# Kernel optimization log

Hardware: AMD Instinct MI355X
Metric: run time of the kernel (lower is better)

Reference implementation:

```python
import jax, jax.numpy as jnp
import numpy as np

N_NODES = 8192
D_FEAT = 256


def setup_inputs() -> dict:
    key = jax.random.key(0)
    k1, k2, k3, k4, k5 = jax.random.split(key, 5)
    X = jax.random.normal(k1, (N_NODES, D_FEAT), dtype=jnp.float32)
    # Dense normalized adjacency-like matrix (A_hat); scale by 1/N for stable magnitudes.
    A_hat = jax.random.uniform(k2, (N_NODES, N_NODES), dtype=jnp.float32) / N_NODES
    w_global = jax.random.uniform(k3, (1,), dtype=jnp.float32)
    w_local = jax.random.uniform(k4, (N_NODES,), dtype=jnp.float32)
    W_agg = jax.random.normal(k5, (D_FEAT, D_FEAT), dtype=jnp.float32) / np.sqrt(D_FEAT)
    return {"X": X, "A_hat": A_hat, "w_global": w_global, "w_local": w_local, "W_agg": W_agg}


def reference(X, A_hat, w_global, w_local, W_agg):
    # GCN-style aggregation: f(X, A_hat) = A_hat @ X @ W_agg, then ReLU.
    agg = jax.nn.relu((A_hat @ X) @ W_agg)  # [n, d]
    # xi = sigmoid(w_global) * diag(sigmoid(w_local)); diagonal => elementwise row scale.
    s = (jax.nn.sigmoid(w_global) * jax.nn.sigmoid(w_local))[:, None]  # [n, 1]
    # xi @ agg + (I - xi) @ X  ==  s*agg + X - s*X, fused in one pass.
    return s * agg + X - s * X
```

## Files before the change

kernel.cpp:

```cpp
#include <hip/hip_runtime.h>
#include <hip/hip_bf16.h>


typedef __attribute__((ext_vector_type(4))) float f32x4;
typedef __attribute__((ext_vector_type(8))) __bf16 bf16x8;
typedef __attribute__((ext_vector_type(8))) unsigned short u16x8;

#define GLOBAL_AS __attribute__((address_space(1)))
#define LDS_AS __attribute__((address_space(3)))

static __device__ __forceinline__ void gload16(const void* g, void* l) {
  __builtin_amdgcn_global_load_lds((const GLOBAL_AS void*)g, (LDS_AS void*)l, 16, 0, 0);
}
static __device__ __forceinline__ void gload16_stream(const void* g, void* l) {
  __builtin_amdgcn_global_load_lds((const GLOBAL_AS void*)g, (LDS_AS void*)l, 16, 0, 0x12);
}

static __device__ __forceinline__ unsigned short f2bf_bits(float f) {
  __bf16 h = (__bf16)f;
  return __builtin_bit_cast(unsigned short, h);
}
static __device__ __forceinline__ float bf2f(unsigned short u) {
  return __builtin_bit_cast(float, (unsigned)u << 16);
}

__global__ void prep_kernel(const float* __restrict__ W,
                            const float* __restrict__ wg,
                            const float* __restrict__ wl,
                            unsigned short* __restrict__ WT,
                            float* __restrict__ s) {
  int tid = blockIdx.x * 256 + threadIdx.x;
  int k = tid >> 8, n = tid & 255;
  float w = W[tid];
  int kt = k >> 5, kloc = k & 31;
  WT[kt * 8192 + n * 32 + kloc] = f2bf_bits(w);
  if (tid < 8192) {
    float sg = 1.0f / (1.0f + expf(-wg[0]));
    float sl = 1.0f / (1.0f + expf(-wl[tid]));
    s[tid] = sg * sl;
  }
}

__global__ __launch_bounds__(256, 2) void gemm_xw(
    const float* __restrict__ X,
    const unsigned short* __restrict__ WT,
    unsigned short* __restrict__ XWT2) {
  __shared__ float As[2][32 * 32];
  __shared__ unsigned short Bs[2][128 * 32];

  const int bm = blockIdx.x & 255;
  const int bn = blockIdx.x >> 8;
  const int m0 = bm * 32;
  const int tid = threadIdx.x;
  const int w = tid >> 6;
  const int l = tid & 63;
  const int lr = l & 15;
  const int lq = l >> 4;

  const int pA = w * 1024 + l * 16;
  const int rA = pA >> 7;
  const int qA = (pA >> 4) & 7;
  const int ssA = qA ^ (rA & 7);
  const char* Asrc0 = (const char*)X + (size_t)(m0 + rA) * 1024 + ssA * 16;
  const char* Bsrc0 = (const char*)WT + bn * 8192 + w * 2048 + l * 16;

  f32x4 acc[2][2];
#pragma unroll
  for (int i = 0; i < 2; ++i)
#pragma unroll
    for (int j = 0; j < 2; ++j) acc[i][j] = (f32x4){0.f, 0.f, 0.f, 0.f};

  auto stage = [&](int t, int buf) {
    gload16(Asrc0 + (size_t)t * 128, (char*)&As[buf][0] + w * 1024);
    const char* bs = Bsrc0 + (size_t)t * 16384;
    gload16(bs, (char*)&Bs[buf][0] + w * 2048);
    gload16(bs + 1024, (char*)&Bs[buf][0] + w * 2048 + 1024);
  };

  auto compute = [&](int buf) {
    bf16x8 af[2];
#pragma unroll
    for (int mi = 0; mi < 2; ++mi) {
      int r = mi * 16 + lr;
      const float* ap = &As[buf][r * 32];
      int s0 = (2 * lq) ^ (r & 7);
      int s1 = (2 * lq + 1) ^ (r & 7);
      f32x4 a0 = *(const f32x4*)(ap + s0 * 4);
      f32x4 a1 = *(const f32x4*)(ap + s1 * 4);
      bf16x8 v;
      v[0] = (__bf16)a0.x; v[1] = (__bf16)a0.y; v[2] = (__bf16)a0.z; v[3] = (__bf16)a0.w;
      v[4] = (__bf16)a1.x; v[5] = (__bf16)a1.y; v[6] = (__bf16)a1.z; v[7] = (__bf16)a1.w;
      af[mi] = v;
    }
    bf16x8 bfr[2];
#pragma unroll
    for (int ni = 0; ni < 2; ++ni) {
      int row = w * 32 + ni * 16 + lr;
      bfr[ni] = *(const bf16x8*)(&Bs[buf][row * 32 + lq * 8]);
    }
#pragma unroll
    for (int mi = 0; mi < 2; ++mi)
#pragma unroll
      for (int ni = 0; ni < 2; ++ni)
        acc[mi][ni] = __builtin_amdgcn_mfma_f32_16x16x32_bf16(af[mi], bfr[ni], acc[mi][ni], 0, 0, 0);
  };

  stage(0, 0);
  __syncthreads();
  for (int t = 0; t < 8; ++t) {
    int cur = t & 1;
    if (t + 1 < 8) stage(t + 1, cur ^ 1);
    compute(cur);
    __syncthreads();
  }

#pragma unroll
  for (int mi = 0; mi < 2; ++mi)
#pragma unroll
    for (int ni2 = 0; ni2 < 2; ++ni2) {
      f32x4 z = acc[mi][ni2];
      int n = bn * 128 + w * 32 + ni2 * 16 + lr;
      int k = bm * 32 + mi * 16 + lq * 4;
      int c = k >> 6;
      int kk = (k >> 5) & 1;
      int ni = (n >> 4) & 1;
      int wp = n >> 5;
      int lane2 = (n & 15) + 16 * ((k >> 3) & 3);
      int j0 = k & 7;
      size_t off = (((size_t)c * 8 + wp) * 4 + kk * 2 + ni) * 512 + lane2 * 8 + j0;
      ushort4 u;
      u.x = f2bf_bits(z[0]); u.y = f2bf_bits(z[1]);
      u.z = f2bf_bits(z[2]); u.w = f2bf_bits(z[3]);
      *(ushort4*)(XWT2 + off) = u;
    }
}

__global__ __launch_bounds__(512, 4) void gemm_ks8(
    const float* __restrict__ A,
    const unsigned short* __restrict__ B2,
    unsigned short* __restrict__ P) {
  __shared__ unsigned short Al[2][8 * 512];

  const int bid = blockIdx.x;
  const int mtile = bid >> 3, kseg = bid & 7;
  const int m0 = mtile * 128;
  const int tid = threadIdx.x;
  const int w = tid >> 6, l = tid & 63;
  const int lr = l & 15, lq = l >> 4;

  const int r = tid >> 2, c4 = tid & 3;
  const float* gA = A + (size_t)(m0 + r) * 8192 + kseg * 1024 + c4 * 8;
  const int woff = (r >> 4) * 512 + ((r & 15) + 16 * c4) * 8;

  const unsigned short* Bbase = B2 + (size_t)kseg * 262144 + l * 8;

  f32x4 acc[8][2];
#pragma unroll
  for (int i = 0; i < 8; ++i)
#pragma unroll
    for (int j = 0; j < 2; ++j) acc[i][j] = (f32x4){0.f, 0.f, 0.f, 0.f};

  f32x4 sa0, sa1;
  bf16x8 Bf0, Bf1;

  auto loadA = [&](int h) {
    sa0 = *(const f32x4*)(gA + h * 32);
    sa1 = *(const f32x4*)(gA + h * 32 + 4);
  };
  auto writeA = [&](int h) {
    bf16x8 b;
    b[0] = (__bf16)sa0.x; b[1] = (__bf16)sa0.y; b[2] = (__bf16)sa0.z; b[3] = (__bf16)sa0.w;
    b[4] = (__bf16)sa1.x; b[5] = (__bf16)sa1.y; b[6] = (__bf16)sa1.z; b[7] = (__bf16)sa1.w;
    *(bf16x8*)(&Al[h & 1][woff]) = b;
  };
  auto loadB = [&](int h) {
    const unsigned short* p = Bbase + ((((h >> 1) * 8 + w) * 4 + (h & 1) * 2) << 9);
    Bf0 = *(const bf16x8*)(p);
    Bf1 = *(const bf16x8*)(p + 512);
  };
  auto compute = [&](int h) {
    const unsigned short* Ab = &Al[h & 1][0];
#pragma unroll
    for (int mi = 0; mi < 8; ++mi) {
      bf16x8 af = *(const bf16x8*)(Ab + mi * 512 + l * 8);
      acc[mi][0] = __builtin_amdgcn_mfma_f32_16x16x32_bf16(af, Bf0, acc[mi][0], 0, 0, 0);
      acc[mi][1] = __builtin_amdgcn_mfma_f32_16x16x32_bf16(af, Bf1, acc[mi][1], 0, 0, 0);
    }
  };

  loadA(0);
  writeA(0);
  loadB(0);
  loadA(1);
  asm volatile("s_waitcnt lgkmcnt(0)" ::: "memory");
  asm volatile("s_barrier" ::: "memory");

  for (int h = 0; h < 31; ++h) {
    compute(h);
    loadB(h + 1);
    writeA(h + 1);
    if (h < 30) loadA(h + 2);
    asm volatile("s_waitcnt lgkmcnt(0)" ::: "memory");
    asm volatile("s_barrier" ::: "memory");
  }
  compute(31);

  unsigned short* Pb = P + (size_t)kseg * (8192 * 256);
#pragma unroll
  for (int mi = 0; mi < 8; ++mi)
#pragma unroll
    for (int ni = 0; ni < 2; ++ni) {
      f32x4 z = acc[mi][ni];
      int n = w * 32 + ni * 16 + lr;
#pragma unroll
      for (int i = 0; i < 4; ++i) {
        int m = m0 + mi * 16 + lq * 4 + i;
        Pb[(size_t)m * 256 + n] = f2bf_bits(z[i]);
      }
    }
}

__global__ __launch_bounds__(256) void finalize8(
    const unsigned short* __restrict__ P,
    const float* __restrict__ X,
    const float* __restrict__ s,
    float* __restrict__ out) {
  int i = blockIdx.x * 256 + threadIdx.x;
  int m = i >> 5;
  float acc[8] = {0.f, 0.f, 0.f, 0.f, 0.f, 0.f, 0.f, 0.f};
#pragma unroll
  for (int ks = 0; ks < 8; ++ks) {
    u16x8 v = *(const u16x8*)(P + (size_t)ks * 2097152 + (size_t)i * 8);
#pragma unroll
    for (int j = 0; j < 8; ++j) acc[j] += bf2f(v[j]);
  }
  float sv = s[m];
  f32x4 x0 = *(const f32x4*)(X + (size_t)i * 8);
  f32x4 x1 = *(const f32x4*)(X + (size_t)i * 8 + 4);
  f32x4 o0, o1;
#pragma unroll
  for (int j = 0; j < 4; ++j) {
    o0[j] = x0[j] + sv * (fmaxf(acc[j], 0.f) - x0[j]);
    o1[j] = x1[j] + sv * (fmaxf(acc[4 + j], 0.f) - x1[j]);
  }
  *(f32x4*)(out + (size_t)i * 8) = o0;
  *(f32x4*)(out + (size_t)i * 8 + 4) = o1;
}

template <int NT, bool SPLIT>
__global__ __launch_bounds__(512, 4) void gemm_main(
    const float* __restrict__ A,
    const unsigned short* __restrict__ B2,
    const float* __restrict__ X,
    const float* __restrict__ s,
    float* __restrict__ out,
    float* __restrict__ P) {
  __shared__ float As[4][32 * 64];

  const int bid = blockIdx.x;
  const int m0 = SPLIT ? (bid >> 1) * 32 : bid * 32;
  const int khalf = SPLIT ? (bid & 1) : 0;
  const int tid = threadIdx.x;
  const int w = tid >> 6;
  const int l = tid & 63;
  const int lr = l & 15;
  const int lq = l >> 4;

  const int rA = tid >> 4;
  const int qA = tid & 15;
  const int sqA = qA ^ (rA & 15);
  const char* Asrc =
      (const char*)A + (size_t)(m0 + rA) * 32768 + (size_t)khalf * 16384 + sqA * 16;
  const char* Bbase =
      (const char*)B2 + (size_t)khalf * 64 * 32768 + (size_t)w * 4096 + (size_t)l * 16;

  f32x4 acc[2][2];
#pragma unroll
  for (int i = 0; i < 2; ++i)
#pragma unroll
    for (int j = 0; j < 2; ++j) acc[i][j] = (f32x4){0.f, 0.f, 0.f, 0.f};

  struct BF { bf16x8 a, b, c, d; };
  BF Bf0, Bf1;

  auto stageA = [&](int h, int buf) {
    gload16_stream(Asrc + (size_t)h * 256, (char*)&As[buf][0] + w * 1024);
  };
  auto loadB = [&](int h, BF& f) {
    const char* p = Bbase + (size_t)h * 32768;
    f.a = *(const bf16x8*)(p);
    f.b = *(const bf16x8*)(p + 1024);
    f.c = *(const bf16x8*)(p + 2048);
    f.d = *(const bf16x8*)(p + 3072);
  };

  auto compute = [&](int buf, const BF& f) {
    const char* Ab = (const char*)&As[buf][0];
    bf16x8 af[2][2];
#pragma unroll
    for (int kk = 0; kk < 2; ++kk)
#pragma unroll
      for (int mi = 0; mi < 2; ++mi) {
        int rr = mi * 16 + lr;
        int s0 = (kk * 8 + 2 * lq) ^ (rr & 15);
        int s1 = ((kk * 8 + 2 * lq) + 1) ^ (rr & 15);
        f32x4 a0 = *(const f32x4*)(Ab + rr * 256 + s0 * 16);
        f32x4 a1 = *(const f32x4*)(Ab + rr * 256 + s1 * 16);
        bf16x8 v;
        v[0] = (__bf16)a0.x; v[1] = (__bf16)a0.y; v[2] = (__bf16)a0.z; v[3] = (__bf16)a0.w;
        v[4] = (__bf16)a1.x; v[5] = (__bf16)a1.y; v[6] = (__bf16)a1.z; v[7] = (__bf16)a1.w;
        af[kk][mi] = v;
      }
    acc[0][0] = __builtin_amdgcn_mfma_f32_16x16x32_bf16(af[0][0], f.a, acc[0][0], 0, 0, 0);
    acc[0][1] = __builtin_amdgcn_mfma_f32_16x16x32_bf16(af[0][0], f.b, acc[0][1], 0, 0, 0);
    acc[1][0] = __builtin_amdgcn_mfma_f32_16x16x32_bf16(af[0][1], f.a, acc[1][0], 0, 0, 0);
    acc[1][1] = __builtin_amdgcn_mfma_f32_16x16x32_bf16(af[0][1], f.b, acc[1][1], 0, 0, 0);
    acc[0][0] = __builtin_amdgcn_mfma_f32_16x16x32_bf16(af[1][0], f.c, acc[0][0], 0, 0, 0);
    acc[0][1] = __builtin_amdgcn_mfma_f32_16x16x32_bf16(af[1][0], f.d, acc[0][1], 0, 0, 0);
    acc[1][0] = __builtin_amdgcn_mfma_f32_16x16x32_bf16(af[1][1], f.c, acc[1][0], 0, 0, 0);
    acc[1][1] = __builtin_amdgcn_mfma_f32_16x16x32_bf16(af[1][1], f.d, acc[1][1], 0, 0, 0);
  };

  stageA(0, 0);
  loadB(0, Bf0);
  stageA(1, 1);
  loadB(1, Bf1);
  stageA(2, 2);
  stageA(3, 3);

  for (int h = 0; h < NT - 4; h += 2) {
    asm volatile("s_waitcnt vmcnt(6)" ::: "memory");
    asm volatile("s_barrier" ::: "memory");
    compute(h & 3, Bf0);
    asm volatile("s_waitcnt lgkmcnt(0)" ::: "memory");
    asm volatile("s_barrier" ::: "memory");
    loadB(h + 2, Bf0);
    stageA(h + 4, h & 3);

    asm volatile("s_waitcnt vmcnt(6)" ::: "memory");
    asm volatile("s_barrier" ::: "memory");
    compute((h + 1) & 3, Bf1);
    asm volatile("s_waitcnt lgkmcnt(0)" ::: "memory");
    asm volatile("s_barrier" ::: "memory");
    loadB(h + 3, Bf1);
    stageA(h + 5, (h + 1) & 3);
  }
  asm volatile("s_waitcnt vmcnt(6)" ::: "memory");
  asm volatile("s_barrier" ::: "memory");
  compute(0, Bf0);
  asm volatile("s_waitcnt lgkmcnt(0)" ::: "memory");
  asm volatile("s_barrier" ::: "memory");
  loadB(NT - 2, Bf0);

  asm volatile("s_waitcnt vmcnt(5)" ::: "memory");
  asm volatile("s_barrier" ::: "memory");
  compute(1, Bf1);
  asm volatile("s_waitcnt lgkmcnt(0)" ::: "memory");
  asm volatile("s_barrier" ::: "memory");
  loadB(NT - 1, Bf1);

  asm volatile("s_waitcnt vmcnt(4)" ::: "memory");
  asm volatile("s_barrier" ::: "memory");
  compute(2, Bf0);
  asm volatile("s_waitcnt lgkmcnt(0)" ::: "memory");
  asm volatile("s_barrier" ::: "memory");

  asm volatile("s_waitcnt vmcnt(0)" ::: "memory");
  asm volatile("s_barrier" ::: "memory");
  compute(3, Bf1);

  if (SPLIT) {
    float* Pb = P + (size_t)khalf * 8192 * 256;
#pragma unroll
    for (int mi = 0; mi < 2; ++mi)
#pragma unroll
      for (int ni = 0; ni < 2; ++ni) {
        f32x4 z = acc[mi][ni];
        int n = w * 32 + ni * 16 + lr;
#pragma unroll
        for (int i = 0; i < 4; ++i) {
          int m = m0 + mi * 16 + lq * 4 + i;
          Pb[m * 256 + n] = z[i];
        }
      }
  } else {
#pragma unroll
    for (int mi = 0; mi < 2; ++mi)
#pragma unroll
      for (int ni = 0; ni < 2; ++ni) {
        f32x4 z = acc[mi][ni];
        int n = w * 32 + ni * 16 + lr;
#pragma unroll
        for (int i = 0; i < 4; ++i) {
          int m = m0 + mi * 16 + lq * 4 + i;
          float x = X[m * 256 + n];
          float sv = s[m];
          out[m * 256 + n] = x + sv * (fmaxf(z[i], 0.f) - x);
        }
      }
  }
}

__global__ __launch_bounds__(256) void finalize_kernel(
    const float* __restrict__ P,
    const float* __restrict__ X,
    const float* __restrict__ s,
    float* __restrict__ out) {
  int i = blockIdx.x * 256 + threadIdx.x;
  int m = i >> 6;
  f32x4 p0 = *(const f32x4*)(P + (size_t)i * 4);
  f32x4 p1 = *(const f32x4*)(P + 2097152 + (size_t)i * 4);
  f32x4 x = *(const f32x4*)(X + (size_t)i * 4);
  float sv = s[m];
  f32x4 o;
#pragma unroll
  for (int j = 0; j < 4; ++j) o[j] = x[j] + sv * (fmaxf(p0[j] + p1[j], 0.f) - x[j]);
  *(f32x4*)(out + (size_t)i * 4) = o;
}

extern "C" void kernel_launch(void* const* d_in, const int* in_sizes, int n_in,
                              void* d_out, int out_size, void* d_ws, size_t ws_size,
                              hipStream_t stream) {
  const float* X = (const float*)d_in[0];
  const float* A = (const float*)d_in[1];
  const float* wg = (const float*)d_in[2];
  const float* wl = (const float*)d_in[3];
  const float* W = (const float*)d_in[4];
  float* out = (float*)d_out;

  unsigned short* XWT2 = (unsigned short*)d_ws;
  unsigned short* WT = (unsigned short*)((char*)d_ws + 4194304);
  float* s = (float*)((char*)d_ws + 4194304 + 131072);
  char* Pbase = (char*)d_ws + 4194304 + 131072 + 32768;

  prep_kernel<<<256, 256, 0, stream>>>(W, wg, wl, WT, s);
  gemm_xw<<<512, 256, 0, stream>>>(X, WT, XWT2);

  const size_t head = 4194304 + 131072 + 32768;
  const size_t need8 = head + (size_t)8 * 8192 * 256 * 2;
  const size_t need2 = head + (size_t)2 * 8192 * 256 * 4;
  if (ws_size >= need8) {
    gemm_ks8<<<512, 512, 0, stream>>>(A, XWT2, (unsigned short*)Pbase);
    finalize8<<<1024, 256, 0, stream>>>((const unsigned short*)Pbase, X, s, out);
  } else if (ws_size >= need2) {
    gemm_main<64, true><<<512, 512, 0, stream>>>(A, XWT2, X, s, out, (float*)Pbase);
    finalize_kernel<<<2048, 256, 0, stream>>>((const float*)Pbase, X, s, out);
  } else {
    gemm_main<128, false><<<256, 512, 0, stream>>>(A, XWT2, X, s, out, nullptr);
  }
}
```

Measured before the change: 103.4 us.

## Double K-step per barrier in split-K GEMM and stagger half the blocks

The split-K GEMM main loop now handles a 64-wide K chunk per iteration instead of 32. It doubles the LDS A tile, gives each thread four float4 loads, and interleaves two half-computes with separate B fragment prefetches, which halves the number of barriers. Separately, blocks with bit 256 of the block index sleep briefly at start, staggering memory traffic. The cost is more LDS and registers per block, which could lower occupancy under launch_bounds(512,4).

```diff
diff --git a/kernel.cpp b/kernel.cpp
--- a/kernel.cpp
+++ b/kernel.cpp
@@ -139,7 +139,7 @@
     const float* __restrict__ A,
     const unsigned short* __restrict__ B2,
     unsigned short* __restrict__ P) {
-  __shared__ unsigned short Al[2][8 * 512];
+  __shared__ unsigned short Al[2][16 * 512];
 
   const int bid = blockIdx.x;
   const int mtile = bid >> 3, kseg = bid & 7;
@@ -148,9 +148,12 @@
   const int w = tid >> 6, l = tid & 63;
   const int lr = l & 15, lq = l >> 4;
 
+  if (bid & 256) __builtin_amdgcn_s_sleep(32);
+
   const int r = tid >> 2, c4 = tid & 3;
-  const float* gA = A + (size_t)(m0 + r) * 8192 + kseg * 1024 + c4 * 8;
-  const int woff = (r >> 4) * 512 + ((r & 15) + 16 * c4) * 8;
+  const float* gA = A + (size_t)(m0 + r) * 8192 + kseg * 1024 + c4 * 16;
+  const int ks = c4 >> 1, kq0 = (c4 & 1) * 2;
+  const int woff0 = (ks * 8 + (r >> 4)) * 512 + ((r & 15) + 16 * kq0) * 8;
 
   const unsigned short* Bbase = B2 + (size_t)kseg * 262144 + l * 8;
 
@@ -160,50 +163,65 @@
 #pragma unroll
     for (int j = 0; j < 2; ++j) acc[i][j] = (f32x4){0.f, 0.f, 0.f, 0.f};
 
-  f32x4 sa0, sa1;
-  bf16x8 Bf0, Bf1;
+  f32x4 sa0, sa1, sa2, sa3;
+  bf16x8 BfA0, BfA1, BfB0, BfB1;
 
   auto loadA = [&](int h) {
-    sa0 = *(const f32x4*)(gA + h * 32);
-    sa1 = *(const f32x4*)(gA + h * 32 + 4);
+    const float* p = gA + h * 64;
+    sa0 = *(const f32x4*)(p);
+    sa1 = *(const f32x4*)(p + 4);
+    sa2 = *(const f32x4*)(p + 8);
+    sa3 = *(const f32x4*)(p + 12);
   };
   auto writeA = [&](int h) {
-    bf16x8 b;
-    b[0] = (__bf16)sa0.x; b[1] = (__bf16)sa0.y; b[2] = (__bf16)sa0.z; b[3] = (__bf16)sa0.w;
-    b[4] = (__bf16)sa1.x; b[5] = (__bf16)sa1.y; b[6] = (__bf16)sa1.z; b[7] = (__bf16)sa1.w;
-    *(bf16x8*)(&Al[h & 1][woff]) = b;
-  };
-  auto loadB = [&](int h) {
-    const unsigned short* p = Bbase + ((((h >> 1) * 8 + w) * 4 + (h & 1) * 2) << 9);
-    Bf0 = *(const bf16x8*)(p);
-    Bf1 = *(const bf16x8*)(p + 512);
-  };
-  auto compute = [&](int h) {
-    const unsigned short* Ab = &Al[h & 1][0];
+    bf16x8 b0, b1;
+    b0[0] = (__bf16)sa0.x; b0[1] = (__bf16)sa0.y; b0[2] = (__bf16)sa0.z; b0[3] = (__bf16)sa0.w;
+    b0[4] = (__bf16)sa1.x; b0[5] = (__bf16)sa1.y; b0[6] = (__bf16)sa1.z; b0[7] = (__bf16)sa1.w;
+    b1[0] = (__bf16)sa2.x; b1[1] = (__bf16)sa2.y; b1[2] = (__bf16)sa2.z; b1[3] = (__bf16)sa2.w;
+    b1[4] = (__bf16)sa3.x; b1[5] = (__bf16)sa3.y; b1[6] = (__bf16)sa3.z; b1[7] = (__bf16)sa3.w;
+    *(bf16x8*)(&Al[h & 1][woff0]) = b0;
+    *(bf16x8*)(&Al[h & 1][woff0 + 128]) = b1;
+  };
+  auto loadBA = [&](int h) {
+    const unsigned short* p = Bbase + (((h * 8 + w) * 4 + 0) << 9);
+    BfA0 = *(const bf16x8*)(p);
+    BfA1 = *(const bf16x8*)(p + 512);
+  };
+  auto loadBB = [&](int h) {
+    const unsigned short* p = Bbase + (((h * 8 + w) * 4 + 2) << 9);
+    BfB0 = *(const bf16x8*)(p);
+    BfB1 = *(const bf16x8*)(p + 512);
+  };
+  auto computeHalf = [&](int buf, int ksel, const bf16x8& F0, const bf16x8& F1) {
+    const unsigned short* Ab = &Al[buf][ksel * 4096];
 #pragma unroll
     for (int mi = 0; mi < 8; ++mi) {
       bf16x8 af = *(const bf16x8*)(Ab + mi * 512 + l * 8);
-      acc[mi][0] = __builtin_amdgcn_mfma_f32_16x16x32_bf16(af, Bf0, acc[mi][0], 0, 0, 0);
-      acc[mi][1] = __builtin_amdgcn_mfma_f32_16x16x32_bf16(af, Bf1, acc[mi][1], 0, 0, 0);
+      acc[mi][0] = __builtin_amdgcn_mfma_f32_16x16x32_bf16(af, F0, acc[mi][0], 0, 0, 0);
+      acc[mi][1] = __builtin_amdgcn_mfma_f32_16x16x32_bf16(af, F1, acc[mi][1], 0, 0, 0);
     }
   };
 
   loadA(0);
   writeA(0);
-  loadB(0);
+  loadBA(0);
+  loadBB(0);
   loadA(1);
   asm volatile("s_waitcnt lgkmcnt(0)" ::: "memory");
   asm volatile("s_barrier" ::: "memory");
 
-  for (int h = 0; h < 31; ++h) {
-    compute(h);
-    loadB(h + 1);
+  for (int h = 0; h < 15; ++h) {
+    computeHalf(h & 1, 0, BfA0, BfA1);
+    loadBA(h + 1);
+    computeHalf(h & 1, 1, BfB0, BfB1);
+    loadBB(h + 1);
     writeA(h + 1);
-    if (h < 30) loadA(h + 2);
+    if (h < 14) loadA(h + 2);
     asm volatile("s_waitcnt lgkmcnt(0)" ::: "memory");
     asm volatile("s_barrier" ::: "memory");
   }
-  compute(31);
+  computeHalf(1, 0, BfA0, BfA1);
+  computeHalf(1, 1, BfB0, BfB1);
 
   unsigned short* Pb = P + (size_t)kseg * (8192 * 256);
 #pragma unroll
```

After: 106.9 us. +3.3%, slower.

## Warp-specialize A@XW GEMM into producer/consumer waves with 8-slot LDS ring

Applied to the files above, without the earlier changes.

Replaces the split-K-by-8 GEMM with a 768-thread kernel where 4 producer waves stream fp32 A with nontemporal loads, convert it to bf16 and fill an 8-slot LDS ring, while 8 consumer waves run MFMAs. Split-K drops from 8 to 4, so the grid is 256 blocks and the bf16 partial buffer and finalize reads are halved. The aim is to overlap A streaming with compute and cut partial-sum traffic. In exchange there are fewer blocks in flight and more LDS and registers per block, and the B operand is now loaded inside the compute step rather than prefetched.

```diff
diff --git a/kernel.cpp b/kernel.cpp
--- a/kernel.cpp
+++ b/kernel.cpp
@@ -135,92 +135,109 @@
     }
 }
 
-__global__ __launch_bounds__(512, 4) void gemm_ks8(
+__global__ __launch_bounds__(768, 3) void gemm_pc(
     const float* __restrict__ A,
     const unsigned short* __restrict__ B2,
     unsigned short* __restrict__ P) {
-  __shared__ unsigned short Al[2][8 * 512];
+  __shared__ unsigned short ring[8 * 4096];
 
   const int bid = blockIdx.x;
-  const int mtile = bid >> 3, kseg = bid & 7;
+  const int mtile = bid >> 2, kseg = bid & 3;
   const int m0 = mtile * 128;
   const int tid = threadIdx.x;
-  const int w = tid >> 6, l = tid & 63;
+  const bool consumer = tid < 512;
+  const int w = tid >> 6;
+  const int l = tid & 63;
   const int lr = l & 15, lq = l >> 4;
 
-  const int r = tid >> 2, c4 = tid & 3;
-  const float* gA = A + (size_t)(m0 + r) * 8192 + kseg * 1024 + c4 * 8;
-  const int woff = (r >> 4) * 512 + ((r & 15) + 16 * c4) * 8;
-
-  const unsigned short* Bbase = B2 + (size_t)kseg * 262144 + l * 8;
-
   f32x4 acc[8][2];
 #pragma unroll
   for (int i = 0; i < 8; ++i)
 #pragma unroll
     for (int j = 0; j < 2; ++j) acc[i][j] = (f32x4){0.f, 0.f, 0.f, 0.f};
 
-  f32x4 sa0, sa1;
-  bf16x8 Bf0, Bf1;
-
-  auto loadA = [&](int h) {
-    sa0 = *(const f32x4*)(gA + h * 32);
-    sa1 = *(const f32x4*)(gA + h * 32 + 4);
-  };
-  auto writeA = [&](int h) {
-    bf16x8 b;
-    b[0] = (__bf16)sa0.x; b[1] = (__bf16)sa0.y; b[2] = (__bf16)sa0.z; b[3] = (__bf16)sa0.w;
-    b[4] = (__bf16)sa1.x; b[5] = (__bf16)sa1.y; b[6] = (__bf16)sa1.z; b[7] = (__bf16)sa1.w;
-    *(bf16x8*)(&Al[h & 1][woff]) = b;
-  };
-  auto loadB = [&](int h) {
-    const unsigned short* p = Bbase + ((((h >> 1) * 8 + w) * 4 + (h & 1) * 2) << 9);
-    Bf0 = *(const bf16x8*)(p);
-    Bf1 = *(const bf16x8*)(p + 512);
-  };
-  auto compute = [&](int h) {
-    const unsigned short* Ab = &Al[h & 1][0];
+  const int p = tid - 512;
+  const int prow = (p & 255) >> 1;
+  const int pk16 = (p & 1) * 16;
+  const float* gA =
+      A + (size_t)(m0 + prow) * 8192 + (size_t)kseg * 2048 + pk16;
+  const int pwoff = (prow >> 4) * 512 + ((prow & 15) + 16 * ((p & 1) * 2)) * 8;
+
+  auto stage_super = [&](int j) {
+    f32x4 v[16];
+#pragma unroll
+    for (int s2 = 0; s2 < 4; ++s2) {
+      const float* src = gA + (size_t)(4 * j + s2) * 32;
+#pragma unroll
+      for (int i = 0; i < 4; ++i)
+        v[s2 * 4 + i] = __builtin_nontemporal_load((const f32x4*)(src + i * 4));
+    }
+#pragma unroll
+    for (int s2 = 0; s2 < 4; ++s2) {
+      int hh = 4 * j + s2;
+      unsigned short* dst = &ring[(hh & 7) * 4096 + pwoff];
+      bf16x8 b0, b1;
+      b0[0] = (__bf16)v[s2 * 4 + 0].x; b0[1] = (__bf16)v[s2 * 4 + 0].y;
+      b0[2] = (__bf16)v[s2 * 4 + 0].z; b0[3] = (__bf16)v[s2 * 4 + 0].w;
+      b0[4] = (__bf16)v[s2 * 4 + 1].x; b0[5] = (__bf16)v[s2 * 4 + 1].y;
+      b0[6] = (__bf16)v[s2 * 4 + 1].z; b0[7] = (__bf16)v[s2 * 4 + 1].w;
+      b1[0] = (__bf16)v[s2 * 4 + 2].x; b1[1] = (__bf16)v[s2 * 4 + 2].y;
+      b1[2] = (__bf16)v[s2 * 4 + 2].z; b1[3] = (__bf16)v[s2 * 4 + 2].w;
+      b1[4] = (__bf16)v[s2 * 4 + 3].x; b1[5] = (__bf16)v[s2 * 4 + 3].y;
+      b1[6] = (__bf16)v[s2 * 4 + 3].z; b1[7] = (__bf16)v[s2 * 4 + 3].w;
+      *(bf16x8*)(dst) = b0;
+      *(bf16x8*)(dst + 128) = b1;
+    }
+  };
+
+  auto compute_slot = [&](int hh) {
+    int c = kseg * 32 + (hh >> 1);
+    const unsigned short* bp =
+        B2 + ((((size_t)c * 8 + w) * 4 + (size_t)(hh & 1) * 2) << 9) + l * 8;
+    bf16x8 B0 = *(const bf16x8*)(bp);
+    bf16x8 B1 = *(const bf16x8*)(bp + 512);
+    const unsigned short* Ab = &ring[(hh & 7) * 4096];
 #pragma unroll
     for (int mi = 0; mi < 8; ++mi) {
       bf16x8 af = *(const bf16x8*)(Ab + mi * 512 + l * 8);
-      acc[mi][0] = __builtin_amdgcn_mfma_f32_16x16x32_bf16(af, Bf0, acc[mi][0], 0, 0, 0);
-      acc[mi][1] = __builtin_amdgcn_mfma_f32_16x16x32_bf16(af, Bf1, acc[mi][1], 0, 0, 0);
-    }
-  };
-
-  loadA(0);
-  writeA(0);
-  loadB(0);
-  loadA(1);
+      acc[mi][0] = __builtin_amdgcn_mfma_f32_16x16x32_bf16(af, B0, acc[mi][0], 0, 0, 0);
+      acc[mi][1] = __builtin_amdgcn_mfma_f32_16x16x32_bf16(af, B1, acc[mi][1], 0, 0, 0);
+    }
+  };
+
+  if (!consumer) stage_super(0);
   asm volatile("s_waitcnt lgkmcnt(0)" ::: "memory");
   asm volatile("s_barrier" ::: "memory");
 
-  for (int h = 0; h < 31; ++h) {
-    compute(h);
-    loadB(h + 1);
-    writeA(h + 1);
-    if (h < 30) loadA(h + 2);
+  for (int sp = 0; sp < 16; ++sp) {
+    if (consumer) {
+#pragma unroll
+      for (int jj = 0; jj < 4; ++jj) compute_slot(sp * 4 + jj);
+    } else {
+      if (sp < 15) stage_super(sp + 1);
+    }
     asm volatile("s_waitcnt lgkmcnt(0)" ::: "memory");
     asm volatile("s_barrier" ::: "memory");
   }
-  compute(31);
-
-  unsigned short* Pb = P + (size_t)kseg * (8192 * 256);
-#pragma unroll
-  for (int mi = 0; mi < 8; ++mi)
-#pragma unroll
-    for (int ni = 0; ni < 2; ++ni) {
-      f32x4 z = acc[mi][ni];
-      int n = w * 32 + ni * 16 + lr;
-#pragma unroll
-      for (int i = 0; i < 4; ++i) {
-        int m = m0 + mi * 16 + lq * 4 + i;
-        Pb[(size_t)m * 256 + n] = f2bf_bits(z[i]);
+
+  if (consumer) {
+    unsigned short* Pb = P + (size_t)kseg * (8192 * 256);
+#pragma unroll
+    for (int mi = 0; mi < 8; ++mi)
+#pragma unroll
+      for (int ni = 0; ni < 2; ++ni) {
+        f32x4 z = acc[mi][ni];
+        int n = w * 32 + ni * 16 + lr;
+#pragma unroll
+        for (int i = 0; i < 4; ++i) {
+          int m = m0 + mi * 16 + lq * 4 + i;
+          Pb[(size_t)m * 256 + n] = f2bf_bits(z[i]);
+        }
       }
-    }
-}
-
-__global__ __launch_bounds__(256) void finalize8(
+  }
+}
+
+__global__ __launch_bounds__(256) void finalize4(
     const unsigned short* __restrict__ P,
     const float* __restrict__ X,
     const float* __restrict__ s,
@@ -229,7 +246,7 @@
   int m = i >> 5;
   float acc[8] = {0.f, 0.f, 0.f, 0.f, 0.f, 0.f, 0.f, 0.f};
 #pragma unroll
-  for (int ks = 0; ks < 8; ++ks) {
+  for (int ks = 0; ks < 4; ++ks) {
     u16x8 v = *(const u16x8*)(P + (size_t)ks * 2097152 + (size_t)i * 8);
 #pragma unroll
     for (int j = 0; j < 8; ++j) acc[j] += bf2f(v[j]);
@@ -437,11 +454,11 @@
   gemm_xw<<<512, 256, 0, stream>>>(X, WT, XWT2);
 
   const size_t head = 4194304 + 131072 + 32768;
-  const size_t need8 = head + (size_t)8 * 8192 * 256 * 2;
+  const size_t need4 = head + (size_t)4 * 8192 * 256 * 2;
   const size_t need2 = head + (size_t)2 * 8192 * 256 * 4;
-  if (ws_size >= need8) {
-    gemm_ks8<<<512, 512, 0, stream>>>(A, XWT2, (unsigned short*)Pbase);
-    finalize8<<<1024, 256, 0, stream>>>((const unsigned short*)Pbase, X, s, out);
+  if (ws_size >= need4) {
+    gemm_pc<<<256, 768, 0, stream>>>(A, XWT2, (unsigned short*)Pbase);
+    finalize4<<<1024, 256, 0, stream>>>((const unsigned short*)Pbase, X, s, out);
   } else if (ws_size >= need2) {
     gemm_main<64, true><<<512, 512, 0, stream>>>(A, XWT2, X, s, out, (float*)Pbase);
     finalize_kernel<<<2048, 256, 0, stream>>>((const float*)Pbase, X, s, out);
```

Result: slower. 131.7 us (+27.3%).

## Fuse split-K reduction into GEMM via last-block atomic counter

Applied to the files above, without the earlier changes.

Removes the separate finalize8 kernel launch. Each split-K block of gemm_ks8 increments a per-mtile atomic counter after writing its partial tile. The last block to arrive reduces the eight bf16 partials and applies the ReLU/sigmoid-blend epilogue. This saves a kernel launch and lets the reductions overlap with still-running GEMM blocks. In exchange, the reduction is serialized onto one block per tile, and it adds threadfences plus counter initialization in the prep kernel.

```diff
diff --git a/kernel.cpp b/kernel.cpp
--- a/kernel.cpp
+++ b/kernel.cpp
@@ -28,7 +28,8 @@
                             const float* __restrict__ wg,
                             const float* __restrict__ wl,
                             unsigned short* __restrict__ WT,
-                            float* __restrict__ s) {
+                            float* __restrict__ s,
+                            int* __restrict__ counters) {
   int tid = blockIdx.x * 256 + threadIdx.x;
   int k = tid >> 8, n = tid & 255;
   float w = W[tid];
@@ -39,6 +40,7 @@
     float sl = 1.0f / (1.0f + expf(-wl[tid]));
     s[tid] = sg * sl;
   }
+  if (tid < 64) counters[tid] = 0;
 }
 
 __global__ __launch_bounds__(256, 2) void gemm_xw(
@@ -138,8 +140,13 @@
 __global__ __launch_bounds__(512, 4) void gemm_ks8(
     const float* __restrict__ A,
     const unsigned short* __restrict__ B2,
-    unsigned short* __restrict__ P) {
+    unsigned short* __restrict__ P,
+    const float* __restrict__ X,
+    const float* __restrict__ s,
+    float* __restrict__ out,
+    int* __restrict__ counters) {
   __shared__ unsigned short Al[2][8 * 512];
+  __shared__ int lastFlag;
 
   const int bid = blockIdx.x;
   const int mtile = bid >> 3, kseg = bid & 7;
@@ -218,33 +225,40 @@
         Pb[(size_t)m * 256 + n] = f2bf_bits(z[i]);
       }
     }
-}
-
-__global__ __launch_bounds__(256) void finalize8(
-    const unsigned short* __restrict__ P,
-    const float* __restrict__ X,
-    const float* __restrict__ s,
-    float* __restrict__ out) {
-  int i = blockIdx.x * 256 + threadIdx.x;
-  int m = i >> 5;
-  float acc[8] = {0.f, 0.f, 0.f, 0.f, 0.f, 0.f, 0.f, 0.f};
-#pragma unroll
-  for (int ks = 0; ks < 8; ++ks) {
-    u16x8 v = *(const u16x8*)(P + (size_t)ks * 2097152 + (size_t)i * 8);
-#pragma unroll
-    for (int j = 0; j < 8; ++j) acc[j] += bf2f(v[j]);
-  }
-  float sv = s[m];
-  f32x4 x0 = *(const f32x4*)(X + (size_t)i * 8);
-  f32x4 x1 = *(const f32x4*)(X + (size_t)i * 8 + 4);
-  f32x4 o0, o1;
-#pragma unroll
-  for (int j = 0; j < 4; ++j) {
-    o0[j] = x0[j] + sv * (fmaxf(acc[j], 0.f) - x0[j]);
-    o1[j] = x1[j] + sv * (fmaxf(acc[4 + j], 0.f) - x1[j]);
-  }
-  *(f32x4*)(out + (size_t)i * 8) = o0;
-  *(f32x4*)(out + (size_t)i * 8 + 4) = o1;
+
+  __threadfence();
+  __syncthreads();
+  if (tid == 0) {
+    int done = atomicAdd(&counters[mtile], 1);
+    lastFlag = (done == 7);
+  }
+  __syncthreads();
+  if (!lastFlag) return;
+
+  __threadfence();
+  for (int g = tid; g < 4096; g += 512) {
+    int mloc = g >> 5;
+    int nd = (g & 31) * 8;
+    int m = m0 + mloc;
+    float accf[8] = {0.f, 0.f, 0.f, 0.f, 0.f, 0.f, 0.f, 0.f};
+#pragma unroll
+    for (int ks = 0; ks < 8; ++ks) {
+      u16x8 v = *(const u16x8*)(P + (size_t)ks * 2097152 + (size_t)m * 256 + nd);
+#pragma unroll
+      for (int j = 0; j < 8; ++j) accf[j] += bf2f(v[j]);
+    }
+    float sv = s[m];
+    f32x4 x0 = *(const f32x4*)(X + (size_t)m * 256 + nd);
+    f32x4 x1 = *(const f32x4*)(X + (size_t)m * 256 + nd + 4);
+    f32x4 o0, o1;
+#pragma unroll
+    for (int j = 0; j < 4; ++j) {
+      o0[j] = x0[j] + sv * (fmaxf(accf[j], 0.f) - x0[j]);
+      o1[j] = x1[j] + sv * (fmaxf(accf[4 + j], 0.f) - x1[j]);
+    }
+    *(f32x4*)(out + (size_t)m * 256 + nd) = o0;
+    *(f32x4*)(out + (size_t)m * 256 + nd + 4) = o1;
+  }
 }
 
 template <int NT, bool SPLIT>
@@ -432,16 +446,18 @@
   unsigned short* WT = (unsigned short*)((char*)d_ws + 4194304);
   float* s = (float*)((char*)d_ws + 4194304 + 131072);
   char* Pbase = (char*)d_ws + 4194304 + 131072 + 32768;
-
-  prep_kernel<<<256, 256, 0, stream>>>(W, wg, wl, WT, s);
+  int* counters = (int*)(Pbase + (size_t)8 * 8192 * 256 * 2);
+
+  const size_t head = 4194304 + 131072 + 32768;
+  const size_t need8 = head + (size_t)8 * 8192 * 256 * 2 + 256;
+  const size_t need2 = head + (size_t)2 * 8192 * 256 * 4;
+
+  prep_kernel<<<256, 256, 0, stream>>>(W, wg, wl, WT, s, counters);
   gemm_xw<<<512, 256, 0, stream>>>(X, WT, XWT2);
 
-  const size_t head = 4194304 + 131072 + 32768;
-  const size_t need8 = head + (size_t)8 * 8192 * 256 * 2;
-  const size_t need2 = head + (size_t)2 * 8192 * 256 * 4;
   if (ws_size >= need8) {
-    gemm_ks8<<<512, 512, 0, stream>>>(A, XWT2, (unsigned short*)Pbase);
-    finalize8<<<1024, 256, 0, stream>>>((const unsigned short*)Pbase, X, s, out);
+    gemm_ks8<<<512, 512, 0, stream>>>(A, XWT2, (unsigned short*)Pbase, X, s, out,
+                                      counters);
   } else if (ws_size >= need2) {
     gemm_main<64, true><<<512, 512, 0, stream>>>(A, XWT2, X, s, out, (float*)Pbase);
     finalize_kernel<<<2048, 256, 0, stream>>>((const float*)Pbase, X, s, out);
```

Measured after the change: 315.7 us. +205.2%, slower.
